# Kernel tuning notes

Hardware: AMD Instinct MI355X
Metric: run time of the kernel (lower is better)

The kernel has to match this reference:

```python
import jax, jax.numpy as jnp
import numpy as np

HEADS = 8
DIM_HEAD = 64
WINDOW = 128
PERSIST = 4
EPS = 1.1920929e-07  # torch nn.RMSNorm default eps = finfo(fp32).eps


def _rope_freqs(n, d, dtype):
    inv_freq = 1.0 / (10000.0 ** (jnp.arange(0, d, 2, dtype=jnp.float32) / d))
    freqs = jnp.arange(n, dtype=jnp.float32)[:, None] * inv_freq[None, :]  # [n, d/2]
    freqs = jnp.repeat(freqs, 2, axis=-1)  # interleaved repeat -> [n, d]
    return jnp.cos(freqs).astype(dtype), jnp.sin(freqs).astype(dtype)


def _rotate_half(x):
    # interleaved pairs (x0,x1),(x2,x3)... -> (-x1,x0),(-x3,x2)...
    x = x.reshape(*x.shape[:-1], -1, 2)
    x1, x2 = x[..., 0], x[..., 1]
    return jnp.stack((-x2, x1), axis=-1).reshape(*x.shape[:-2], -1)


def setup_inputs() -> dict:
    key = jax.random.key(0)
    k1, k2, k3 = jax.random.split(key, 3)
    B, N, D = 1, 4096, 1024
    dim_inner = HEADS * DIM_HEAD  # 512
    return {
        "seq": jax.random.normal(k1, (B, N, D), dtype=jnp.float32),
        "g": jnp.ones((D,), dtype=jnp.float32),
        "w_qkv": jax.random.normal(k2, (D, 3 * dim_inner), dtype=jnp.float32) * 0.02,
        "w_out": jax.random.normal(k3, (dim_inner, D), dtype=jnp.float32) * 0.02,
    }


def reference(seq, g, w_qkv, w_out):
    B, N, D = seq.shape
    H, Dh = HEADS, DIM_HEAD

    # RMSNorm
    x = seq * jax.lax.rsqrt(jnp.mean(seq * seq, axis=-1, keepdims=True) + EPS) * g

    # QKV projection -> [B, H, N, Dh]
    qkv = x @ w_qkv
    q, k, v = jnp.split(qkv, 3, axis=-1)
    to_heads = lambda t: t.reshape(B, N, H, Dh).transpose(0, 2, 1, 3)
    q, k, v = map(to_heads, (q, k, v))

    # rotary embeddings (same positions for q and k)
    cos, sin = _rope_freqs(N, Dh, q.dtype)
    q = q * cos + _rotate_half(q) * sin
    k = k * cos + _rotate_half(k) * sin

    # causal & (persist | sliding-window) mask
    idx = jnp.arange(N)
    dist = idx[:, None] - idx[None, :]
    mask = (dist >= 0) & ((idx[None, :] < PERSIST) | (dist <= WINDOW))  # [N, N]

    scale = Dh ** -0.5
    scores = jnp.einsum("bhid,bhjd->bhij", q, k) * scale
    neg = -jnp.finfo(scores.dtype).max
    scores = jnp.where(mask[None, None], scores, neg)
    attn = jax.nn.softmax(scores, axis=-1)
    out = jnp.einsum("bhij,bhjd->bhid", attn, v)

    out = out.transpose(0, 2, 1, 3).reshape(B, N, H * Dh)
    return out @ w_out
```

## Files before the change

kernel.cpp:

```cpp
#include <hip/hip_runtime.h>
#include <hip/hip_bf16.h>
#include <math.h>

#define SEQ    4096
#define DMODEL 1024
#define NHEADS 8
#define DH     64
#define DINNER 512
#define NQKV   1536
#define WINDOW 128
#define PERSIST 4
#define EPS 1.1920929e-07f

typedef unsigned short u16;
typedef unsigned int   u32;
typedef __bf16  bf16_8 __attribute__((ext_vector_type(8)));
typedef float   f32x4  __attribute__((ext_vector_type(4)));

union BV { bf16_8 v; u16 s[8]; };

__device__ __forceinline__ float b2f(u16 u) {
    union { u32 i; float f; } v; v.i = ((u32)u) << 16; return v.f;
}
__device__ __forceinline__ u16 f2b(float f) {
    union { float f; u32 i; } v; v.f = f;
    u32 i = v.i;
    u32 r = (i + 0x7fffu + ((i >> 16) & 1u)) >> 16;
    return (u16)r;
}

#define GLD16(gp, lp) __builtin_amdgcn_global_load_lds( \
    (const __attribute__((address_space(1))) void*)(gp), \
    (__attribute__((address_space(3))) void*)(lp), 16, 0, 0)

__global__ __launch_bounds__(256) void transpose_kernel(const float* __restrict__ src,
                                                        u16* __restrict__ dst,
                                                        int K, int N) {
    __shared__ u16 t[64][65];
    int bn = blockIdx.x * 64, bk = blockIdx.y * 64;
    int tid = threadIdx.x;
    int r = tid >> 4, c4 = (tid & 15) * 4;
    #pragma unroll
    for (int it = 0; it < 4; it++) {
        int row = r + it * 16;
        float4 v = *(const float4*)(src + (size_t)(bk + row) * N + bn + c4);
        t[row][c4 + 0] = f2b(v.x);
        t[row][c4 + 1] = f2b(v.y);
        t[row][c4 + 2] = f2b(v.z);
        t[row][c4 + 3] = f2b(v.w);
    }
    __syncthreads();
    #pragma unroll
    for (int it = 0; it < 4; it++) {
        int n = r + it * 16;
        u16* d = dst + (size_t)(bn + n) * K + bk + c4;
        d[0] = t[c4 + 0][n];
        d[1] = t[c4 + 1][n];
        d[2] = t[c4 + 2][n];
        d[3] = t[c4 + 3][n];
    }
}

__global__ __launch_bounds__(256) void rmsnorm_kernel(const float* __restrict__ seq,
                                                      const float* __restrict__ g,
                                                      u16* __restrict__ x) {
    int row = blockIdx.x, tid = threadIdx.x;
    float4 v = *(const float4*)(seq + (size_t)row * DMODEL + tid * 4);
    float ss = v.x*v.x + v.y*v.y + v.z*v.z + v.w*v.w;
    #pragma unroll
    for (int o = 32; o > 0; o >>= 1) ss += __shfl_xor(ss, o);
    __shared__ float wsum[4];
    if ((tid & 63) == 0) wsum[tid >> 6] = ss;
    __syncthreads();
    float tot = wsum[0] + wsum[1] + wsum[2] + wsum[3];
    float rstd = rsqrtf(tot * (1.0f / DMODEL) + EPS);
    float4 gv = *(const float4*)(g + tid * 4);
    uint2 o;
    o.x = (u32)f2b(v.x * rstd * gv.x) | ((u32)f2b(v.y * rstd * gv.y) << 16);
    o.y = (u32)f2b(v.z * rstd * gv.z) | ((u32)f2b(v.w * rstd * gv.w) << 16);
    *(uint2*)(x + (size_t)row * DMODEL + tid * 4) = o;
}

template <int MODE>
__global__ __launch_bounds__(256, 2) void gemm2_kernel(const u16* __restrict__ A,
                                                       const u16* __restrict__ Bt,
                                                       u16* __restrict__ C0,
                                                       u16* __restrict__ C1,
                                                       u16* __restrict__ C2,
                                                       float* __restrict__ Cf,
                                                       int M, int N, int K) {
    __shared__ u16 As[128 * 64];
    __shared__ u16 Bs[128 * 64];
    int bx = blockIdx.x, by = blockIdx.y, tid = threadIdx.x;
    int lane = tid & 63, wave = tid >> 6;
    int m16 = lane & 15, quad = lane >> 4;
    int rw0 = (wave & 1) * 64, cw0 = (wave >> 1) * 64;

    f32x4 acc[4][4];
    #pragma unroll
    for (int mt = 0; mt < 4; mt++)
        #pragma unroll
        for (int nt = 0; nt < 4; nt++) acc[mt][nt] = (f32x4){0.f, 0.f, 0.f, 0.f};

    int lrow = lane & 7, lkc = lane >> 3;
    const u16* Ag = A  + (size_t)(by * 128 + lrow) * K + lkc * 8;
    const u16* Bg = Bt + (size_t)(bx * 128 + lrow) * K + lkc * 8;

    for (int k0 = 0; k0 < K; k0 += 64) {
        #pragma unroll
        for (int r = 0; r < 4; r++) {
            int g = wave * 4 + r;
            GLD16(Ag + (size_t)(g * 8) * K + k0, As + g * 512);
            GLD16(Bg + (size_t)(g * 8) * K + k0, Bs + g * 512);
        }
        __syncthreads();

        #pragma unroll
        for (int kk = 0; kk < 2; kk++) {
            int kc = kk * 4 + quad;
            bf16_8 afr[4], bfr[4];
            #pragma unroll
            for (int mt = 0; mt < 4; mt++) {
                int row = rw0 + mt * 16 + m16;
                afr[mt] = *(const bf16_8*)(As + (row >> 3) * 512 + kc * 64 + (row & 7) * 8);
            }
            #pragma unroll
            for (int nt = 0; nt < 4; nt++) {
                int col = cw0 + nt * 16 + m16;
                bfr[nt] = *(const bf16_8*)(Bs + (col >> 3) * 512 + kc * 64 + (col & 7) * 8);
            }
            #pragma unroll
            for (int mt = 0; mt < 4; mt++)
                #pragma unroll
                for (int nt = 0; nt < 4; nt++)
                    acc[mt][nt] = __builtin_amdgcn_mfma_f32_16x16x32_bf16(afr[mt], bfr[nt], acc[mt][nt], 0, 0, 0);
        }
        __syncthreads();
    }

    #pragma unroll
    for (int mt = 0; mt < 4; mt++) {
        #pragma unroll
        for (int nt = 0; nt < 4; nt++) {
            #pragma unroll
            for (int r = 0; r < 4; r++) {
                int row = by * 128 + rw0 + mt * 16 + quad * 4 + r;
                int col = bx * 128 + cw0 + nt * 16 + m16;
                if (MODE == 0) {
                    int tens = col >> 9, hh = (col >> 6) & 7, dh = col & 63;
                    u16* dst = (tens == 0) ? C0 : ((tens == 1) ? C1 : C2);
                    dst[((size_t)hh * SEQ + row) * DH + dh] = f2b(acc[mt][nt][r]);
                } else {
                    Cf[(size_t)row * N + col] = acc[mt][nt][r];
                }
            }
        }
    }
}

__global__ __launch_bounds__(256) void rope_kernel(u16* __restrict__ Q, u16* __restrict__ Kt) {
    int idx = blockIdx.x * 256 + threadIdx.x;
    int tensor = idx >> 20;
    int r = idx & 0xfffff;
    int t = r & 31;
    int n = (r >> 5) & 4095;
    int h = r >> 17;
    u16* p = (tensor == 0 ? Q : Kt) + ((size_t)h * SEQ + n) * DH + 2 * t;
    float e = (float)(2 * t) / 64.0f;
    float inv = exp2f(-e * 13.287712379549449f);
    float ang = (float)n * inv;
    float s, c;
    sincosf(ang, &s, &c);
    float x0 = b2f(p[0]), x1 = b2f(p[1]);
    p[0] = f2b(x0 * c - x1 * s);
    p[1] = f2b(x1 * c + x0 * s);
}

#define AROWS 208
#define KLD   72
#define PLD   168

__global__ __launch_bounds__(256, 2) void attn_mfma(const u16* __restrict__ Q,
                                                    const u16* __restrict__ Kt,
                                                    const u16* __restrict__ V,
                                                    u16* __restrict__ O) {
    __shared__ u16 Ks[AROWS * KLD];
    __shared__ u16 Vs[AROWS * 64];
    __shared__ u16 Ps[4 * 16 * PLD];
    int i0 = blockIdx.x * 64, h = blockIdx.y;
    int tid = threadIdx.x, wave = tid >> 6, lane = tid & 63;
    int m16 = lane & 15, quad = lane >> 4;
    int smin = (i0 > WINDOW) ? i0 - WINDOW : 0;

    for (int idx = tid; idx < AROWS * 8; idx += 256) {
        int row = idx >> 3, c = idx & 7;
        int j = (row < 16) ? row : (smin + row - 16);
        size_t goff = ((size_t)h * SEQ + j) * DH + c * 8;
        *(bf16_8*)(Ks + row * KLD + c * 8) = *(const bf16_8*)(Kt + goff);
        int swz = (row ^ (row >> 3)) & 7;
        *(bf16_8*)(Vs + row * 64 + ((c ^ swz) << 3)) = *(const bf16_8*)(V + goff);
    }

    int iw0 = i0 + wave * 16;
    int iq = iw0 + m16;
    const u16* qrow = Q + ((size_t)h * SEQ + iq) * DH;
    bf16_8 qa = *(const bf16_8*)(qrow + quad * 8);
    bf16_8 qb = *(const bf16_8*)(qrow + 32 + quad * 8);
    __syncthreads();

    int start_w = (iw0 > WINDOW) ? iw0 - WINDOW : 0;
    int Dw = start_w - smin;
    int tlast = 31 + iw0 - start_w;
    int nch = (tlast >> 4) + 1;
    int nk32 = (tlast >> 5) + 1;

    f32x4 S[10];
    #pragma unroll
    for (int c = 0; c < 10; c++) {
        if (c < nch) {
            int t = c * 16 + m16;
            int row = (c == 0) ? t : (t + Dw);
            const u16* kp = Ks + row * KLD;
            bf16_8 kb0 = *(const bf16_8*)(kp + quad * 8);
            bf16_8 kb1 = *(const bf16_8*)(kp + 32 + quad * 8);
            f32x4 s = (f32x4){0.f, 0.f, 0.f, 0.f};
            s = __builtin_amdgcn_mfma_f32_16x16x32_bf16(qa, kb0, s, 0, 0, 0);
            s = __builtin_amdgcn_mfma_f32_16x16x32_bf16(qb, kb1, s, 0, 0, 0);
            S[c] = s;
        }
    }

    float mrow[4] = {-1e30f, -1e30f, -1e30f, -1e30f};
    #pragma unroll
    for (int c = 0; c < 10; c++) {
        if (c < nch) {
            int t = c * 16 + m16;
            int j = (c == 0) ? t : (start_w + t - 16);
            #pragma unroll
            for (int r = 0; r < 4; r++) {
                int i = iw0 + quad * 4 + r;
                bool valid = (c == 0) ? (j < PERSIST && j < start_w)
                                      : (j <= i && (i - j <= WINDOW || j < PERSIST));
                float sv = valid ? S[c][r] * 0.125f : -1e30f;
                S[c][r] = sv;
                mrow[r] = fmaxf(mrow[r], sv);
            }
        }
    }
    #pragma unroll
    for (int r = 0; r < 4; r++) {
        #pragma unroll
        for (int o = 1; o < 16; o <<= 1) mrow[r] = fmaxf(mrow[r], __shfl_xor(mrow[r], o));
    }
    float srow[4] = {0.f, 0.f, 0.f, 0.f};
    #pragma unroll
    for (int c = 0; c < 10; c++) {
        if (c < nch) {
            #pragma unroll
            for (int r = 0; r < 4; r++) {
                float p = expf(S[c][r] - mrow[r]);
                S[c][r] = p;
                srow[r] += p;
            }
        }
    }
    #pragma unroll
    for (int r = 0; r < 4; r++) {
        #pragma unroll
        for (int o = 1; o < 16; o <<= 1) srow[r] += __shfl_xor(srow[r], o);
    }

    u16* pw = Ps + wave * 16 * PLD;
    #pragma unroll
    for (int c = 0; c < 10; c++) {
        #pragma unroll
        for (int r = 0; r < 4; r++) {
            u16 val = (c < nch) ? f2b(S[c][r]) : (u16)0;
            pw[(quad * 4 + r) * PLD + c * 16 + m16] = val;
        }
    }

    f32x4 oacc[4];
    #pragma unroll
    for (int nt = 0; nt < 4; nt++) oacc[nt] = (f32x4){0.f, 0.f, 0.f, 0.f};
    #pragma unroll
    for (int c2 = 0; c2 < 5; c2++) {
        if (c2 < nk32) {
            bf16_8 af = *(const bf16_8*)(pw + m16 * PLD + c2 * 32 + quad * 8);
            #pragma unroll
            for (int nt = 0; nt < 4; nt++) {
                union BV bv;
                int d = nt * 16 + m16;
                #pragma unroll
                for (int jj = 0; jj < 8; jj++) {
                    int k = c2 * 32 + quad * 8 + jj;
                    int row = (k < 16) ? k : (k + Dw);
                    int swz = (row ^ (row >> 3)) & 7;
                    bv.s[jj] = Vs[row * 64 + ((((d >> 3) ^ swz) << 3) | (d & 7))];
                }
                oacc[nt] = __builtin_amdgcn_mfma_f32_16x16x32_bf16(af, bv.v, oacc[nt], 0, 0, 0);
            }
        }
    }

    #pragma unroll
    for (int nt = 0; nt < 4; nt++) {
        #pragma unroll
        for (int r = 0; r < 4; r++) {
            int i = iw0 + quad * 4 + r;
            O[(size_t)i * DINNER + h * DH + nt * 16 + m16] = f2b(oacc[nt][r] / srow[r]);
        }
    }
}

extern "C" void kernel_launch(void* const* d_in, const int* in_sizes, int n_in,
                              void* d_out, int out_size, void* d_ws, size_t ws_size,
                              hipStream_t stream) {
    const float* seq  = (const float*)d_in[0];
    const float* g    = (const float*)d_in[1];
    const float* wqkv = (const float*)d_in[2];
    const float* wout = (const float*)d_in[3];
    float* out = (float*)d_out;

    char* ws = (char*)d_ws;
    u16* x       = (u16*)(ws);
    u16* q       = (u16*)(ws + 8ll  * 1024 * 1024);
    u16* k       = (u16*)(ws + 12ll * 1024 * 1024);
    u16* v       = (u16*)(ws + 16ll * 1024 * 1024);
    u16* att     = (u16*)(ws + 20ll * 1024 * 1024);
    u16* wqkv_bt = (u16*)(ws + 24ll * 1024 * 1024);
    u16* wout_bt = (u16*)(ws + 27ll * 1024 * 1024);

    dim3 t1(NQKV / 64, DMODEL / 64);
    transpose_kernel<<<t1, 256, 0, stream>>>(wqkv, wqkv_bt, DMODEL, NQKV);
    dim3 t2(DMODEL / 64, DINNER / 64);
    transpose_kernel<<<t2, 256, 0, stream>>>(wout, wout_bt, DINNER, DMODEL);

    rmsnorm_kernel<<<SEQ, 256, 0, stream>>>(seq, g, x);

    dim3 g1(NQKV / 128, SEQ / 128);
    gemm2_kernel<0><<<g1, 256, 0, stream>>>(x, wqkv_bt, q, k, v, nullptr, SEQ, NQKV, DMODEL);

    rope_kernel<<<(2 * 1048576) / 256, 256, 0, stream>>>(q, k);

    dim3 g2(SEQ / 64, NHEADS);
    attn_mfma<<<g2, 256, 0, stream>>>(q, k, v, att);

    dim3 g3(DMODEL / 128, SEQ / 128);
    gemm2_kernel<1><<<g3, 256, 0, stream>>>(att, wout_bt, nullptr, nullptr, nullptr, out, SEQ, DMODEL, DINNER);
}
```

Measured before the change: 154.5 us.

## Fuse prep kernels, fold RoPE into QKV GEMM epilogue, transpose V in LDS

Combines the two weight transposes and RMSNorm into one launch, and applies rotary embedding inside the QKV GEMM epilogue using a lane shuffle to fetch the pair partner. This drops the separate rope kernel and its read-modify-write pass over Q and K. The attention kernel now stores V transposed in LDS so each PV operand is a single vector load instead of eight scalar gathers. K and P share LDS behind a new barrier, which lowers LDS use. The trade-off is more per-element sincos work in the GEMM epilogue and strided scalar stores when writing the transposed V.

```diff
diff --git a/kernel.cpp b/kernel.cpp
--- a/kernel.cpp
+++ b/kernel.cpp
@@ -33,12 +33,10 @@
     (const __attribute__((address_space(1))) void*)(gp), \
     (__attribute__((address_space(3))) void*)(lp), 16, 0, 0)
 
-__global__ __launch_bounds__(256) void transpose_kernel(const float* __restrict__ src,
-                                                        u16* __restrict__ dst,
-                                                        int K, int N) {
-    __shared__ u16 t[64][65];
-    int bn = blockIdx.x * 64, bk = blockIdx.y * 64;
-    int tid = threadIdx.x;
+__device__ __forceinline__ void transpose_tile(const float* __restrict__ src,
+                                               u16* __restrict__ dst,
+                                               int K, int N, int bn, int bk,
+                                               u16 (*t)[65], int tid) {
     int r = tid >> 4, c4 = (tid & 15) * 4;
     #pragma unroll
     for (int it = 0; it < 4; it++) {
@@ -61,24 +59,37 @@
     }
 }
 
-__global__ __launch_bounds__(256) void rmsnorm_kernel(const float* __restrict__ seq,
-                                                      const float* __restrict__ g,
-                                                      u16* __restrict__ x) {
-    int row = blockIdx.x, tid = threadIdx.x;
-    float4 v = *(const float4*)(seq + (size_t)row * DMODEL + tid * 4);
-    float ss = v.x*v.x + v.y*v.y + v.z*v.z + v.w*v.w;
-    #pragma unroll
-    for (int o = 32; o > 0; o >>= 1) ss += __shfl_xor(ss, o);
+__global__ __launch_bounds__(256) void prep_kernel(const float* __restrict__ wqkv,
+                                                   const float* __restrict__ wout,
+                                                   const float* __restrict__ seq,
+                                                   const float* __restrict__ g,
+                                                   u16* __restrict__ wqkv_bt,
+                                                   u16* __restrict__ wout_bt,
+                                                   u16* __restrict__ x) {
+    __shared__ u16 t[64][65];
     __shared__ float wsum[4];
-    if ((tid & 63) == 0) wsum[tid >> 6] = ss;
-    __syncthreads();
-    float tot = wsum[0] + wsum[1] + wsum[2] + wsum[3];
-    float rstd = rsqrtf(tot * (1.0f / DMODEL) + EPS);
-    float4 gv = *(const float4*)(g + tid * 4);
-    uint2 o;
-    o.x = (u32)f2b(v.x * rstd * gv.x) | ((u32)f2b(v.y * rstd * gv.y) << 16);
-    o.y = (u32)f2b(v.z * rstd * gv.z) | ((u32)f2b(v.w * rstd * gv.w) << 16);
-    *(uint2*)(x + (size_t)row * DMODEL + tid * 4) = o;
+    int b = blockIdx.x, tid = threadIdx.x;
+    if (b < 384) {
+        transpose_tile(wqkv, wqkv_bt, DMODEL, NQKV, (b % 24) * 64, (b / 24) * 64, t, tid);
+    } else if (b < 512) {
+        int bb = b - 384;
+        transpose_tile(wout, wout_bt, DINNER, DMODEL, (bb % 16) * 64, (bb / 16) * 64, t, tid);
+    } else {
+        int row = b - 512;
+        float4 v = *(const float4*)(seq + (size_t)row * DMODEL + tid * 4);
+        float ss = v.x*v.x + v.y*v.y + v.z*v.z + v.w*v.w;
+        #pragma unroll
+        for (int o = 32; o > 0; o >>= 1) ss += __shfl_xor(ss, o);
+        if ((tid & 63) == 0) wsum[tid >> 6] = ss;
+        __syncthreads();
+        float tot = wsum[0] + wsum[1] + wsum[2] + wsum[3];
+        float rstd = rsqrtf(tot * (1.0f / DMODEL) + EPS);
+        float4 gv = *(const float4*)(g + tid * 4);
+        uint2 o;
+        o.x = (u32)f2b(v.x * rstd * gv.x) | ((u32)f2b(v.y * rstd * gv.y) << 16);
+        o.y = (u32)f2b(v.z * rstd * gv.z) | ((u32)f2b(v.w * rstd * gv.w) << 16);
+        *(uint2*)(x + (size_t)row * DMODEL + tid * 4) = o;
+    }
 }
 
 template <int MODE>
@@ -109,9 +120,9 @@
     for (int k0 = 0; k0 < K; k0 += 64) {
         #pragma unroll
         for (int r = 0; r < 4; r++) {
-            int g = wave * 4 + r;
-            GLD16(Ag + (size_t)(g * 8) * K + k0, As + g * 512);
-            GLD16(Bg + (size_t)(g * 8) * K + k0, Bs + g * 512);
+            int gg = wave * 4 + r;
+            GLD16(Ag + (size_t)(gg * 8) * K + k0, As + gg * 512);
+            GLD16(Bg + (size_t)(gg * 8) * K + k0, Bs + gg * 512);
         }
         __syncthreads();
 
@@ -139,54 +150,57 @@
     }
 
     #pragma unroll
-    for (int mt = 0; mt < 4; mt++) {
-        #pragma unroll
-        for (int nt = 0; nt < 4; nt++) {
-            #pragma unroll
-            for (int r = 0; r < 4; r++) {
-                int row = by * 128 + rw0 + mt * 16 + quad * 4 + r;
-                int col = bx * 128 + cw0 + nt * 16 + m16;
-                if (MODE == 0) {
-                    int tens = col >> 9, hh = (col >> 6) & 7, dh = col & 63;
-                    u16* dst = (tens == 0) ? C0 : ((tens == 1) ? C1 : C2);
-                    dst[((size_t)hh * SEQ + row) * DH + dh] = f2b(acc[mt][nt][r]);
-                } else {
+    for (int nt = 0; nt < 4; nt++) {
+        int col = bx * 128 + cw0 + nt * 16 + m16;
+        if (MODE == 0) {
+            int tt = (col & 63) >> 1;
+            float inv = exp2f(-(float)(2 * tt) * (13.287712379549449f / 64.0f));
+            bool isv = (col >= 2 * DINNER);
+            bool odd = (col & 1);
+            int tens = col >> 9, hh = (col >> 6) & 7, dh = col & 63;
+            u16* dst = (tens == 0) ? C0 : ((tens == 1) ? C1 : C2);
+            #pragma unroll
+            for (int mt = 0; mt < 4; mt++) {
+                #pragma unroll
+                for (int r = 0; r < 4; r++) {
+                    int row = by * 128 + rw0 + mt * 16 + quad * 4 + r;
+                    float own = acc[mt][nt][r];
+                    float part = __shfl_xor(own, 1);
+                    float val = own;
+                    if (!isv) {
+                        float s, c;
+                        __sincosf((float)row * inv, &s, &c);
+                        val = odd ? (own * c + part * s) : (own * c - part * s);
+                    }
+                    dst[((size_t)hh * SEQ + row) * DH + dh] = f2b(val);
+                }
+            }
+        } else {
+            #pragma unroll
+            for (int mt = 0; mt < 4; mt++) {
+                #pragma unroll
+                for (int r = 0; r < 4; r++) {
+                    int row = by * 128 + rw0 + mt * 16 + quad * 4 + r;
                     Cf[(size_t)row * N + col] = acc[mt][nt][r];
                 }
             }
         }
     }
-}
-
-__global__ __launch_bounds__(256) void rope_kernel(u16* __restrict__ Q, u16* __restrict__ Kt) {
-    int idx = blockIdx.x * 256 + threadIdx.x;
-    int tensor = idx >> 20;
-    int r = idx & 0xfffff;
-    int t = r & 31;
-    int n = (r >> 5) & 4095;
-    int h = r >> 17;
-    u16* p = (tensor == 0 ? Q : Kt) + ((size_t)h * SEQ + n) * DH + 2 * t;
-    float e = (float)(2 * t) / 64.0f;
-    float inv = exp2f(-e * 13.287712379549449f);
-    float ang = (float)n * inv;
-    float s, c;
-    sincosf(ang, &s, &c);
-    float x0 = b2f(p[0]), x1 = b2f(p[1]);
-    p[0] = f2b(x0 * c - x1 * s);
-    p[1] = f2b(x1 * c + x0 * s);
 }
 
 #define AROWS 208
 #define KLD   72
 #define PLD   168
+#define VLD   222
 
 __global__ __launch_bounds__(256, 2) void attn_mfma(const u16* __restrict__ Q,
                                                     const u16* __restrict__ Kt,
                                                     const u16* __restrict__ V,
                                                     u16* __restrict__ O) {
-    __shared__ u16 Ks[AROWS * KLD];
-    __shared__ u16 Vs[AROWS * 64];
-    __shared__ u16 Ps[4 * 16 * PLD];
+    __shared__ __align__(16) char smem[29952 + 64 * VLD * 2];
+    u16* Ks = (u16*)smem;
+    u16* Ps = (u16*)smem;
+    u16* Vt = (u16*)(smem + 29952);
     int i0 = blockIdx.x * 64, h = blockIdx.y;
     int tid = threadIdx.x, wave = tid >> 6, lane = tid & 63;
     int m16 = lane & 15, quad = lane >> 4;
@@ -197,8 +211,9 @@
         int j = (row < 16) ? row : (smin + row - 16);
         size_t goff = ((size_t)h * SEQ + j) * DH + c * 8;
         *(bf16_8*)(Ks + row * KLD + c * 8) = *(const bf16_8*)(Kt + goff);
-        int swz = (row ^ (row >> 3)) & 7;
-        *(bf16_8*)(Vs + row * 64 + ((c ^ swz) << 3)) = *(const bf16_8*)(V + goff);
+        union BV u; u.v = *(const bf16_8*)(V + goff);
+        #pragma unroll
+        for (int e = 0; e < 8; e++) Vt[(c * 8 + e) * VLD + row] = u.s[e];
     }
 
     int iw0 = i0 + wave * 16;
@@ -229,6 +244,7 @@
             S[c] = s;
         }
     }
+    __syncthreads();
 
     float mrow[4] = {-1e30f, -1e30f, -1e30f, -1e30f};
     #pragma unroll
@@ -287,18 +303,13 @@
     for (int c2 = 0; c2 < 5; c2++) {
         if (c2 < nk32) {
             bf16_8 af = *(const bf16_8*)(pw + m16 * PLD + c2 * 32 + quad * 8);
+            int kbase = c2 * 32 + quad * 8;
+            int rowb = (kbase < 16) ? kbase : (kbase + Dw);
             #pragma unroll
             for (int nt = 0; nt < 4; nt++) {
-                union BV bv;
                 int d = nt * 16 + m16;
-                #pragma unroll
-                for (int jj = 0; jj < 8; jj++) {
-                    int k = c2 * 32 + quad * 8 + jj;
-                    int row = (k < 16) ? k : (k + Dw);
-                    int swz = (row ^ (row >> 3)) & 7;
-                    bv.s[jj] = Vs[row * 64 + ((((d >> 3) ^ swz) << 3) | (d & 7))];
-                }
-                oacc[nt] = __builtin_amdgcn_mfma_f32_16x16x32_bf16(af, bv.v, oacc[nt], 0, 0, 0);
+                bf16_8 bv = *(const bf16_8*)(Vt + d * VLD + rowb);
+                oacc[nt] = __builtin_amdgcn_mfma_f32_16x16x32_bf16(af, bv, oacc[nt], 0, 0, 0);
             }
         }
     }
@@ -331,18 +342,11 @@
     u16* wqkv_bt = (u16*)(ws + 24ll * 1024 * 1024);
     u16* wout_bt = (u16*)(ws + 27ll * 1024 * 1024);
 
-    dim3 t1(NQKV / 64, DMODEL / 64);
-    transpose_kernel<<<t1, 256, 0, stream>>>(wqkv, wqkv_bt, DMODEL, NQKV);
-    dim3 t2(DMODEL / 64, DINNER / 64);
-    transpose_kernel<<<t2, 256, 0, stream>>>(wout, wout_bt, DINNER, DMODEL);
-
-    rmsnorm_kernel<<<SEQ, 256, 0, stream>>>(seq, g, x);
+    prep_kernel<<<4608, 256, 0, stream>>>(wqkv, wout, seq, g, wqkv_bt, wout_bt, x);
 
     dim3 g1(NQKV / 128, SEQ / 128);
     gemm2_kernel<0><<<g1, 256, 0, stream>>>(x, wqkv_bt, q, k, v, nullptr, SEQ, NQKV, DMODEL);
 
-    rope_kernel<<<(2 * 1048576) / 256, 256, 0, stream>>>(q, k);
-
     dim3 g2(SEQ / 64, NHEADS);
     attn_mfma<<<g2, 256, 0, stream>>>(q, k, v, att);
 
```

New measurement: 146.8 us. 1.05x faster.
